# Kernel optimization log

Hardware: AMD Instinct MI355X
Metric: run time of the kernel (lower is better)

The kernel has to match this reference:

```python
import jax, jax.numpy as jnp
import numpy as np

# Qwen3-0.6B-like config; 4 equal-length requests flattened into [R*S, H]
L, R, S, H = 2, 4, 1024, 1024
NH, NKV, DH = 16, 8, 128
FF = 3072
EPS = 1e-6
THETA = 1e6
SCALE = 0.02  # weight init scale to keep activations sane


def setup_inputs() -> dict:
    key = jax.random.key(0)
    ks = jax.random.split(key, 8)
    return {
        "hidden_states": jax.random.normal(ks[0], (R * S, H), jnp.float32),
        "Wq": jax.random.normal(ks[1], (L, H, NH * DH), jnp.float32) * SCALE,
        "Wk": jax.random.normal(ks[2], (L, H, NKV * DH), jnp.float32) * SCALE,
        "Wv": jax.random.normal(ks[3], (L, H, NKV * DH), jnp.float32) * SCALE,
        "Wo": jax.random.normal(ks[4], (L, NH * DH, H), jnp.float32) * SCALE,
        "q_norm_w": jnp.ones((L, DH), jnp.float32),
        "k_norm_w": jnp.ones((L, DH), jnp.float32),
        "ln1_w": jnp.ones((L, H), jnp.float32),
        "ln2_w": jnp.ones((L, H), jnp.float32),
        "Wg": jax.random.normal(ks[5], (L, H, FF), jnp.float32) * SCALE,
        "Wu": jax.random.normal(ks[6], (L, H, FF), jnp.float32) * SCALE,
        "Wd": jax.random.normal(ks[7], (L, FF, H), jnp.float32) * SCALE,
        "final_norm_w": jnp.ones((H,), jnp.float32),
    }


def _rms(x, w):
    return x * jax.lax.rsqrt(jnp.mean(x * x, axis=-1, keepdims=True) + EPS) * w


def _rope_tables():
    inv_freq = 1.0 / (THETA ** (jnp.arange(0, DH, 2, dtype=jnp.float32) / DH))
    pos = jnp.arange(S, dtype=jnp.float32)  # per-request positions 0..S-1 (prefill)
    freqs = pos[:, None] * inv_freq[None, :]        # [S, DH/2]
    emb = jnp.concatenate([freqs, freqs], axis=-1)  # [S, DH]
    return jnp.cos(emb), jnp.sin(emb)


def _rotate_half(x):
    x1, x2 = jnp.split(x, 2, axis=-1)
    return jnp.concatenate([-x2, x1], axis=-1)


def _apply_rope(x, cos, sin):
    # x: [R, heads, S, DH]; cos/sin: [S, DH]
    c = cos[None, None]
    s = sin[None, None]
    return x * c + _rotate_half(x) * s


def reference(hidden_states, Wq, Wk, Wv, Wo, q_norm_w, k_norm_w, ln1_w, ln2_w,
              Wg, Wu, Wd, final_norm_w):
    cos, sin = _rope_tables()
    causal = jnp.tril(jnp.ones((S, S), dtype=bool))  # per-request causal mask
    neg = jnp.finfo(hidden_states.dtype).min
    scaling = 1.0 / jnp.sqrt(jnp.asarray(DH, hidden_states.dtype))

    x = hidden_states
    for l in range(L):
        # --- attention block ---
        residual = x
        h = _rms(x, ln1_w[l])                       # [R*S, H]
        q = (h @ Wq[l]).reshape(R, S, NH, DH)
        k = (h @ Wk[l]).reshape(R, S, NKV, DH)
        v = (h @ Wv[l]).reshape(R, S, NKV, DH)
        q = _rms(q, q_norm_w[l]).transpose(0, 2, 1, 3)   # [R, NH, S, DH]
        k = _rms(k, k_norm_w[l]).transpose(0, 2, 1, 3)   # [R, NKV, S, DH]
        v = v.transpose(0, 2, 1, 3)                      # [R, NKV, S, DH]
        q = _apply_rope(q, cos, sin)
        k = _apply_rope(k, cos, sin)
        # GQA: repeat KV heads
        rep = NH // NKV
        k = jnp.repeat(k, rep, axis=1)
        v = jnp.repeat(v, rep, axis=1)
        scores = jnp.einsum('rhqd,rhkd->rhqk', q, k) * scaling
        scores = jnp.where(causal[None, None], scores, neg)
        attn = jax.nn.softmax(scores, axis=-1)
        o = jnp.einsum('rhqk,rhkd->rhqd', attn, v)       # [R, NH, S, DH]
        o = o.transpose(0, 2, 1, 3).reshape(R * S, NH * DH)
        x = residual + o @ Wo[l]
        # --- MLP block ---
        residual = x
        h = _rms(x, ln2_w[l])
        x = residual + (jax.nn.silu(h @ Wg[l]) * (h @ Wu[l])) @ Wd[l]
    return _rms(x, final_norm_w)
```

## Files before the change

kernel.cpp:

```cpp
#include <hip/hip_runtime.h>
#include <hip/hip_bf16.h>

typedef __bf16 bf16;
typedef __bf16 bf16x8 __attribute__((ext_vector_type(8)));
typedef float f32x4 __attribute__((ext_vector_type(4)));

#define DEVINL __device__ __forceinline__

constexpr int L_ = 2, R_ = 4, S_ = 1024, H_ = 1024;
constexpr int NH_ = 16, NKV_ = 8, DH_ = 128;
constexpr int FF_ = 3072;
constexpr int T_ = R_ * S_;

DEVINL void gload16(const bf16* g, bf16* l) {
    __builtin_amdgcn_global_load_lds(
        (const __attribute__((address_space(1))) void*)g,
        (__attribute__((address_space(3))) void*)l, 16, 0, 0);
}

__global__ void rope_tables_kernel(float* __restrict__ cosb, float* __restrict__ sinb) {
    int s = blockIdx.x;
    int i = threadIdx.x;
    float inv = __expf(-(float)i * (1.0f / 64.0f) * 13.815510557964274f);
    float f = (float)s * inv;
    cosb[s * 64 + i] = cosf(f);
    sinb[s * 64 + i] = sinf(f);
}

template <bool OUT_BF16>
__global__ __launch_bounds__(256) void rmsnorm_kernel(const float* __restrict__ x,
                                                      const float* __restrict__ w,
                                                      void* __restrict__ out) {
    int row = blockIdx.x;
    const float* xr = x + (size_t)row * H_;
    int t = threadIdx.x;
    float v[4];
    float ss = 0.f;
#pragma unroll
    for (int j = 0; j < 4; ++j) {
        v[j] = xr[t + 256 * j];
        ss += v[j] * v[j];
    }
#pragma unroll
    for (int off = 32; off; off >>= 1) ss += __shfl_xor(ss, off);
    __shared__ float part[4];
    if ((t & 63) == 0) part[t >> 6] = ss;
    __syncthreads();
    ss = part[0] + part[1] + part[2] + part[3];
    float r = rsqrtf(ss * (1.0f / (float)H_) + 1e-6f);
#pragma unroll
    for (int j = 0; j < 4; ++j) {
        int c = t + 256 * j;
        float o = v[j] * r * w[c];
        if constexpr (OUT_BF16)
            ((bf16*)out)[(size_t)row * H_ + c] = (bf16)o;
        else
            ((float*)out)[(size_t)row * H_ + c] = o;
    }
}

__global__ __launch_bounds__(256) void transpose_cast_kernel(const float* __restrict__ in,
                                                             bf16* __restrict__ out,
                                                             int Rk, int Cn, int mode) {
    __shared__ float tile[32][33];
    int c0 = blockIdx.x * 32, r0 = blockIdx.y * 32;
    int t = threadIdx.x;
    int tc = t & 31, tr = t >> 5;
#pragma unroll
    for (int i = 0; i < 4; ++i) {
        int r = tr + i * 8;
        tile[r][tc] = in[(size_t)(r0 + r) * Cn + c0 + tc];
    }
    __syncthreads();
#pragma unroll
    for (int i = 0; i < 4; ++i) {
        int c = c0 + tr + i * 8;
        int n = (mode == 0) ? c : (((c >> 4) << 5) + ((mode == 2) ? 16 : 0) + (c & 15));
        out[(size_t)n * Rk + r0 + tc] = (bf16)tile[tc][tr + i * 8];
    }
}

__global__ __launch_bounds__(256) void vt_kernel(const bf16* __restrict__ qkv,
                                                 bf16* __restrict__ vt) {
    __shared__ bf16 tile[32][34];
    int s0 = blockIdx.x * 32, c0 = blockIdx.y * 32, r = blockIdx.z;
    int t = threadIdx.x, tc = t & 31, tr = t >> 5;
#pragma unroll
    for (int i = 0; i < 4; ++i) {
        int s = tr + i * 8;
        tile[s][tc] = qkv[(size_t)(r * 1024 + s0 + s) * 4096 + 3072 + c0 + tc];
    }
    __syncthreads();
#pragma unroll
    for (int i = 0; i < 4; ++i) {
        int c = tr + i * 8;
        vt[((size_t)(r * 1024 + c0 + c)) * 1024 + s0 + tc] = tile[tc][c];
    }
}

template <int EPI>
__global__ __launch_bounds__(512, 4) void gemmP_kernel(const bf16* __restrict__ A,
                                                       const bf16* __restrict__ Bt,
                                                       void* __restrict__ out,
                                                       int M, int N, int K) {
    __shared__ bf16 lds[36864];
    const int NT = K >> 5;
    int nbn = N >> 8;
    int nwg = (M >> 7) * nbn;
    int id = blockIdx.x;
    int sid = (id & 7) * (nwg >> 3) + (id >> 3);
    int bm = (sid / nbn) << 7, bn = (sid % nbn) << 8;
    int t = threadIdx.x, lane = t & 63, w = t >> 6;
    int wm = w >> 2, wn = w & 3;
    int hi = lane >> 4, f = lane & 15;

    int srow = t >> 2;
    int ssc = (t & 3) ^ ((srow >> 1) & 3);
    const bf16* aSrc = A + (size_t)(bm + srow) * K + (ssc << 3);
    const bf16* b0Src = Bt + (size_t)(bn + srow) * K + (ssc << 3);
    const bf16* b1Src = Bt + (size_t)(bn + 128 + srow) * K + (ssc << 3);

    f32x4 acc[4][4] = {};

    auto stage = [&](int tt, int sb) {
        gload16(aSrc + tt * 32, lds + sb * 4096 + w * 512);
        gload16(b0Src + tt * 32, lds + 12288 + sb * 8192 + w * 512);
        gload16(b1Src + tt * 32, lds + 12288 + sb * 8192 + 4096 + w * 512);
    };

    stage(0, 0);
    stage(1, 1);
    asm volatile("s_waitcnt vmcnt(3)" ::: "memory");
    __builtin_amdgcn_s_barrier();

    int cb = 0;
    for (int tau = 0; tau < NT; ++tau) {
        const bf16* aB = lds + cb * 4096;
        const bf16* bB = lds + 12288 + cb * 8192;
        if (tau + 2 < NT) stage(tau + 2, (cb == 0) ? 2 : cb - 1);
        bf16x8 af[4], bfv[4];
#pragma unroll
        for (int mf = 0; mf < 4; ++mf) {
            int row = wm * 64 + mf * 16 + f;
            af[mf] = *(const bf16x8*)(aB + row * 32 + ((hi ^ ((row >> 1) & 3)) << 3));
        }
#pragma unroll
        for (int nf = 0; nf < 4; ++nf) {
            int row = wn * 64 + nf * 16 + f;
            bfv[nf] = *(const bf16x8*)(bB + row * 32 + ((hi ^ ((row >> 1) & 3)) << 3));
        }
        __builtin_amdgcn_s_setprio(1);
#pragma unroll
        for (int mf = 0; mf < 4; ++mf)
#pragma unroll
            for (int nf = 0; nf < 4; ++nf)
                acc[mf][nf] = __builtin_amdgcn_mfma_f32_16x16x32_bf16(af[mf], bfv[nf],
                                                                      acc[mf][nf], 0, 0, 0);
        __builtin_amdgcn_s_setprio(0);
        if (tau < NT - 2)
            asm volatile("s_waitcnt vmcnt(3)" ::: "memory");
        else
            asm volatile("s_waitcnt vmcnt(0)" ::: "memory");
        __builtin_amdgcn_s_barrier();
        cb = (cb == 2) ? 0 : cb + 1;
    }

    int rb = bm + wm * 64 + hi * 4;
#pragma unroll
    for (int mf = 0; mf < 4; ++mf) {
        if constexpr (EPI == 5) {
#pragma unroll
            for (int p = 0; p < 2; ++p) {
                int col = ((bn + wn * 64) >> 1) + p * 16 + f;
#pragma unroll
                for (int g = 0; g < 4; ++g) {
                    float gv = acc[mf][2 * p][g], uv = acc[mf][2 * p + 1][g];
                    float sv = gv / (1.0f + __expf(-gv));
                    ((bf16*)out)[(size_t)(rb + mf * 16 + g) * (N / 2) + col] = (bf16)(sv * uv);
                }
            }
        } else {
            int cb2 = bn + wn * 64 + f;
#pragma unroll
            for (int nf = 0; nf < 4; ++nf)
#pragma unroll
                for (int g = 0; g < 4; ++g)
                    ((bf16*)out)[(size_t)(rb + mf * 16 + g) * N + cb2 + nf * 16] =
                        (bf16)acc[mf][nf][g];
        }
    }
}

template <int EPI, int BM>
__global__ __launch_bounds__(256) void gemm_kernel(const bf16* __restrict__ A,
                                                   const bf16* __restrict__ Bt,
                                                   void* __restrict__ out,
                                                   const float* __restrict__ res,
                                                   int M, int N, int K) {
    constexpr int MF = BM / 32;
    __shared__ bf16 Al[BM * 32];
    __shared__ bf16 Bl[128 * 32];
    int gx = gridDim.x;
    int nwg = gx * gridDim.y;
    int id = blockIdx.y * gx + blockIdx.x;
    int sid = (id & 7) * (nwg >> 3) + (id >> 3);
    int bm = (sid / gx) * BM, bn = (sid % gx) * 128;
    int t = threadIdx.x;
    int lane = t & 63, w = t >> 6;
    int wr = w >> 1, wc = w & 1;
    f32x4 acc[MF][4] = {};

    int srow = t >> 2, scol = (t & 3) * 8;
    const bf16* Ap = A + (size_t)(bm + srow) * K + scol;
    const bf16* Bp = Bt + (size_t)(bn + srow) * K + scol;
    bf16* Adst = Al + w * 512;
    bf16* Bdst = Bl + w * 512;

    int kl = (lane >> 4) * 8;
    int rm = wr * (BM / 2) + (lane & 15);
    int rn = wc * 64 + (lane & 15);

    for (int k0 = 0; k0 < K; k0 += 32) {
        __syncthreads();
        gload16(Ap, Adst);
        if constexpr (BM == 128) gload16(Ap + (size_t)64 * K, Adst + 2048);
        gload16(Bp, Bdst);
        gload16(Bp + (size_t)64 * K, Bdst + 2048);
        Ap += 32;
        Bp += 32;
        __syncthreads();
        bf16x8 af[MF], bfv[4];
#pragma unroll
        for (int m = 0; m < MF; ++m) af[m] = *(const bf16x8*)(Al + (rm + m * 16) * 32 + kl);
#pragma unroll
        for (int n = 0; n < 4; ++n) bfv[n] = *(const bf16x8*)(Bl + (rn + n * 16) * 32 + kl);
#pragma unroll
        for (int m = 0; m < MF; ++m)
#pragma unroll
            for (int n = 0; n < 4; ++n)
                acc[m][n] = __builtin_amdgcn_mfma_f32_16x16x32_bf16(af[m], bfv[n], acc[m][n], 0, 0, 0);
    }

    int f = lane & 15;
    int rbase = bm + wr * (BM / 2) + ((lane >> 4) << 2);
    int cbase = bn + wc * 64 + f;
#pragma unroll
    for (int m = 0; m < MF; ++m) {
#pragma unroll
        for (int n = 0; n < 4; ++n) {
#pragma unroll
            for (int g = 0; g < 4; ++g) {
                int row = rbase + m * 16 + g;
                size_t idx = (size_t)row * N + cbase + n * 16;
                ((float*)out)[idx] = acc[m][n][g] + res[idx];
            }
        }
    }
}

DEVINL void head_norm_rope(const bf16* __restrict__ src, const float* __restrict__ w,
                           const float* __restrict__ cosb, const float* __restrict__ sinb,
                           int s, int ln, bf16* __restrict__ dst) {
    float x0 = (float)src[ln], x1 = (float)src[ln + 32];
    float x2 = (float)src[ln + 64], x3 = (float)src[ln + 96];
    float ss = x0 * x0 + x1 * x1 + x2 * x2 + x3 * x3;
#pragma unroll
    for (int off = 16; off; off >>= 1) ss += __shfl_xor(ss, off);
    float rr = rsqrtf(ss * (1.0f / 128.0f) + 1e-6f);
    float n0 = x0 * rr * w[ln], n1 = x1 * rr * w[ln + 32];
    float n2 = x2 * rr * w[ln + 64], n3 = x3 * rr * w[ln + 96];
    float c0 = cosb[s * 64 + ln], c1 = cosb[s * 64 + ln + 32];
    float s0 = sinb[s * 64 + ln], s1 = sinb[s * 64 + ln + 32];
    dst[ln] = (bf16)(n0 * c0 - n2 * s0);
    dst[ln + 32] = (bf16)(n1 * c1 - n3 * s1);
    dst[ln + 64] = (bf16)(n2 * c0 + n0 * s0);
    dst[ln + 96] = (bf16)(n3 * c1 + n1 * s1);
}

__global__ __launch_bounds__(256) void qkv_post_kernel(const bf16* __restrict__ qkv,
                                                       const float* __restrict__ qw,
                                                       const float* __restrict__ kw,
                                                       const float* __restrict__ cosb,
                                                       const float* __restrict__ sinb,
                                                       bf16* __restrict__ qo,
                                                       bf16* __restrict__ ko) {
    int tok = blockIdx.x;
    int r = tok >> 10, s = tok & 1023;
    int t = threadIdx.x;
    int g = t >> 5;
    int ln = t & 31;
    const bf16* row = qkv + (size_t)tok * 4096;
#pragma unroll
    for (int hh = 0; hh < 2; ++hh) {
        int h = g + hh * 8;
        head_norm_rope(row + h * 128, qw, cosb, sinb, s, ln,
                       qo + ((size_t)(r * NH_ + h) * S_ + s) * 128);
    }
    head_norm_rope(row + 2048 + g * 128, kw, cosb, sinb, s, ln,
                   ko + ((size_t)(r * NKV_ + g) * S_ + s) * 128);
}

__global__ __launch_bounds__(256, 2) void flash_kernel(const bf16* __restrict__ q,
                                                       const bf16* __restrict__ k,
                                                       const bf16* __restrict__ vt,
                                                       bf16* __restrict__ out) {
    __shared__ bf16 Kl[64 * 128];
    __shared__ bf16 Vl[128 * 64];
    __shared__ bf16 Pl[4][32][72];
    int bid = blockIdx.x;
    int grp = bid & 63, slot = bid >> 6;
    int strip = (slot < 4) ? (7 - slot) : (slot - 4);
    int h = 2 * (grp & 7) + ((grp >> 3) & 1);
    int r = grp >> 4;
    int kvh = h >> 1;

    int t = threadIdx.x, lane = t & 63, w = t >> 6;
    int arow = lane & 15, hi = lane >> 4;
    int a7 = arow & 7;
    int grow = hi * 4;
    int qbase = strip * 128 + w * 32;

    const bf16* qp = q + ((size_t)(r * NH_ + h) * S_ + qbase) * 128;
    bf16x8 qf[2][4];
#pragma unroll
    for (int m = 0; m < 2; ++m)
#pragma unroll
        for (int kc = 0; kc < 4; ++kc)
            qf[m][kc] = *(const bf16x8*)(qp + (size_t)(m * 16 + arow) * 128 + kc * 32 + hi * 8);

    const bf16* kp = k + (size_t)(r * NKV_ + kvh) * S_ * 128;
    const bf16* vp = vt + (size_t)(r * NKV_ + kvh) * 128 * S_;

    int krow0 = t >> 4, kc16 = t & 15;
    int vrow0 = t >> 3, vc16 = t & 7;

    f32x4 ao[2][8] = {};
    float mrow[2][4], lrow[2][4];
#pragma unroll
    for (int m = 0; m < 2; ++m)
#pragma unroll
        for (int g = 0; g < 4; ++g) { mrow[m][g] = -1e30f; lrow[m][g] = 0.f; }
    const float scale = 0.08838834764831845f;

    int nt = 2 * (strip + 1);
    bf16x8 krs[4], vrs[4];
#pragma unroll
    for (int i = 0; i < 4; ++i)
        krs[i] = *(const bf16x8*)(kp + (size_t)(krow0 + 16 * i) * 128 + kc16 * 8);
#pragma unroll
    for (int i = 0; i < 4; ++i)
        vrs[i] = *(const bf16x8*)(vp + (size_t)(vrow0 + 32 * i) * S_ + vc16 * 8);

    for (int it = 0; it < nt; ++it) {
        int kv0 = it * 64;
        __syncthreads();
#pragma unroll
        for (int i = 0; i < 4; ++i) {
            int row = krow0 + 16 * i;
            *(bf16x8*)(&Kl[row * 128 + ((kc16 ^ (row & 7)) * 8)]) = krs[i];
        }
#pragma unroll
        for (int i = 0; i < 4; ++i) {
            int row = vrow0 + 32 * i;
            *(bf16x8*)(&Vl[row * 64 + ((vc16 ^ (row & 7)) * 8)]) = vrs[i];
        }
        __syncthreads();
        if (it + 1 < nt) {
            int kvn = kv0 + 64;
#pragma unroll
            for (int i = 0; i < 4; ++i)
                krs[i] = *(const bf16x8*)(kp + (size_t)(kvn + krow0 + 16 * i) * 128 + kc16 * 8);
#pragma unroll
            for (int i = 0; i < 4; ++i)
                vrs[i] = *(const bf16x8*)(vp + (size_t)(vrow0 + 32 * i) * S_ + kvn + vc16 * 8);
        }
        f32x4 sc[2][4];
#pragma unroll
        for (int m = 0; m < 2; ++m)
#pragma unroll
            for (int n = 0; n < 4; ++n) sc[m][n] = (f32x4){0.f, 0.f, 0.f, 0.f};
#pragma unroll
        for (int n = 0; n < 4; ++n) {
            int krw = n * 16 + arow;
#pragma unroll
            for (int kc = 0; kc < 4; ++kc) {
                bf16x8 kf = *(const bf16x8*)(&Kl[krw * 128 + (((kc * 4 + hi) ^ a7) * 8)]);
                sc[0][n] = __builtin_amdgcn_mfma_f32_16x16x32_bf16(qf[0][kc], kf, sc[0][n], 0, 0, 0);
                sc[1][n] = __builtin_amdgcn_mfma_f32_16x16x32_bf16(qf[1][kc], kf, sc[1][n], 0, 0, 0);
            }
        }
#pragma unroll
        for (int m = 0; m < 2; ++m) {
            float pm[4][4];
            bool msk = (kv0 + 64 > qbase + m * 16);
#pragma unroll
            for (int n = 0; n < 4; ++n)
#pragma unroll
                for (int g = 0; g < 4; ++g) {
                    float sval = sc[m][n][g] * scale;
                    if (msk && (kv0 + n * 16 + arow > qbase + m * 16 + grow + g)) sval = -1e30f;
                    pm[n][g] = sval;
                }
            float mx[4], sf[4], rs[4];
#pragma unroll
            for (int g = 0; g < 4; ++g)
                mx[g] = fmaxf(fmaxf(pm[0][g], pm[1][g]), fmaxf(pm[2][g], pm[3][g]));
#pragma unroll
            for (int off = 8; off; off >>= 1)
#pragma unroll
                for (int g = 0; g < 4; ++g) mx[g] = fmaxf(mx[g], __shfl_xor(mx[g], off));
#pragma unroll
            for (int g = 0; g < 4; ++g) {
                float mnew = fmaxf(mrow[m][g], mx[g]);
                sf[g] = __expf(mrow[m][g] - mnew);
                mrow[m][g] = mnew;
            }
#pragma unroll
            for (int n = 0; n < 4; ++n)
#pragma unroll
                for (int g = 0; g < 4; ++g) pm[n][g] = __expf(pm[n][g] - mrow[m][g]);
#pragma unroll
            for (int g = 0; g < 4; ++g) rs[g] = pm[0][g] + pm[1][g] + pm[2][g] + pm[3][g];
#pragma unroll
            for (int off = 8; off; off >>= 1)
#pragma unroll
                for (int g = 0; g < 4; ++g) rs[g] += __shfl_xor(rs[g], off);
#pragma unroll
            for (int g = 0; g < 4; ++g) lrow[m][g] = lrow[m][g] * sf[g] + rs[g];
#pragma unroll
            for (int c = 0; c < 8; ++c)
#pragma unroll
                for (int g = 0; g < 4; ++g) ao[m][c][g] *= sf[g];
#pragma unroll
            for (int n = 0; n < 4; ++n)
#pragma unroll
                for (int g = 0; g < 4; ++g)
                    Pl[w][m * 16 + grow + g][n * 16 + arow] = (bf16)pm[n][g];
        }
        bf16x8 pf[2][2];
#pragma unroll
        for (int m = 0; m < 2; ++m)
#pragma unroll
            for (int ks = 0; ks < 2; ++ks)
                pf[m][ks] = *(const bf16x8*)(&Pl[w][m * 16 + arow][ks * 32 + hi * 8]);
#pragma unroll
        for (int c = 0; c < 8; ++c) {
            int vrw = c * 16 + arow;
#pragma unroll
            for (int ks = 0; ks < 2; ++ks) {
                bf16x8 vf = *(const bf16x8*)(&Vl[vrw * 64 + (((ks * 4 + hi) ^ a7) * 8)]);
                ao[0][c] = __builtin_amdgcn_mfma_f32_16x16x32_bf16(pf[0][ks], vf, ao[0][c], 0, 0, 0);
                ao[1][c] = __builtin_amdgcn_mfma_f32_16x16x32_bf16(pf[1][ks], vf, ao[1][c], 0, 0, 0);
            }
        }
    }
#pragma unroll
    for (int m = 0; m < 2; ++m)
#pragma unroll
        for (int c = 0; c < 8; ++c)
#pragma unroll
            for (int g = 0; g < 4; ++g) {
                int rq = qbase + m * 16 + grow + g;
                out[(size_t)(r * S_ + rq) * 2048 + h * 128 + c * 16 + arow] =
                    (bf16)(ao[m][c][g] / lrow[m][g]);
            }
}

extern "C" void kernel_launch(void* const* d_in, const int* in_sizes, int n_in,
                              void* d_out, int out_size, void* d_ws, size_t ws_size,
                              hipStream_t stream) {
    const float* hidden = (const float*)d_in[0];
    const float* Wq = (const float*)d_in[1];
    const float* Wk = (const float*)d_in[2];
    const float* Wv = (const float*)d_in[3];
    const float* Wo = (const float*)d_in[4];
    const float* qnw = (const float*)d_in[5];
    const float* knw = (const float*)d_in[6];
    const float* ln1 = (const float*)d_in[7];
    const float* ln2 = (const float*)d_in[8];
    const float* Wg = (const float*)d_in[9];
    const float* Wu = (const float*)d_in[10];
    const float* Wd = (const float*)d_in[11];
    const float* fnw = (const float*)d_in[12];
    float* out = (float*)d_out;

    char* ws = (char*)d_ws;
    size_t off = 0;
    auto alloc = [&](size_t bytes) -> char* {
        char* p = ws + off;
        off += (bytes + 255) & ~(size_t)255;
        return p;
    };
    float* cosb = (float*)alloc((size_t)S_ * 64 * 4);
    float* sinb = (float*)alloc((size_t)S_ * 64 * 4);
    float* x_ws = (float*)alloc((size_t)T_ * H_ * 4);
    bf16* hbuf = (bf16*)alloc((size_t)T_ * H_ * 2);
    bf16* qkv = (bf16*)alloc((size_t)T_ * 4096 * 2);
    bf16* act = qkv;
    bf16* qb = (bf16*)alloc((size_t)R_ * NH_ * S_ * 128 * 2);
    bf16* kb = (bf16*)alloc((size_t)R_ * NKV_ * S_ * 128 * 2);
    bf16* vtb = (bf16*)alloc((size_t)R_ * NKV_ * 128 * S_ * 2);
    bf16* attn = (bf16*)alloc((size_t)T_ * 2048 * 2);
    bf16* wqkv_t = (bf16*)alloc((size_t)4096 * 1024 * 2);
    bf16* wo_t = (bf16*)alloc((size_t)1024 * 2048 * 2);
    bf16* wgu_t = (bf16*)alloc((size_t)6144 * 1024 * 2);
    bf16* wd_t = (bf16*)alloc((size_t)1024 * 3072 * 2);

    rope_tables_kernel<<<S_, 64, 0, stream>>>(cosb, sinb);

    const float* xin = hidden;
    for (int l = 0; l < L_; ++l) {
        transpose_cast_kernel<<<dim3(2048 / 32, 1024 / 32), 256, 0, stream>>>(
            Wq + (size_t)l * H_ * 2048, wqkv_t, 1024, 2048, 0);
        transpose_cast_kernel<<<dim3(1024 / 32, 1024 / 32), 256, 0, stream>>>(
            Wk + (size_t)l * H_ * 1024, wqkv_t + (size_t)2048 * 1024, 1024, 1024, 0);
        transpose_cast_kernel<<<dim3(1024 / 32, 1024 / 32), 256, 0, stream>>>(
            Wv + (size_t)l * H_ * 1024, wqkv_t + (size_t)3072 * 1024, 1024, 1024, 0);
        transpose_cast_kernel<<<dim3(1024 / 32, 2048 / 32), 256, 0, stream>>>(
            Wo + (size_t)l * 2048 * 1024, wo_t, 2048, 1024, 0);
        transpose_cast_kernel<<<dim3(3072 / 32, 1024 / 32), 256, 0, stream>>>(
            Wg + (size_t)l * H_ * 3072, wgu_t, 1024, 3072, 1);
        transpose_cast_kernel<<<dim3(3072 / 32, 1024 / 32), 256, 0, stream>>>(
            Wu + (size_t)l * H_ * 3072, wgu_t, 1024, 3072, 2);
        transpose_cast_kernel<<<dim3(1024 / 32, 3072 / 32), 256, 0, stream>>>(
            Wd + (size_t)l * 3072 * 1024, wd_t, 3072, 1024, 0);

        rmsnorm_kernel<true><<<T_, 256, 0, stream>>>(xin, ln1 + (size_t)l * H_, hbuf);
        gemmP_kernel<1><<<512, 512, 0, stream>>>(hbuf, wqkv_t, qkv, 4096, 4096, 1024);
        qkv_post_kernel<<<T_, 256, 0, stream>>>(qkv, qnw + (size_t)l * 128, knw + (size_t)l * 128,
                                                cosb, sinb, qb, kb);
        vt_kernel<<<dim3(32, 32, 4), 256, 0, stream>>>(qkv, vtb);
        flash_kernel<<<512, 256, 0, stream>>>(qb, kb, vtb, attn);
        gemm_kernel<4, 64><<<dim3(8, 64), 256, 0, stream>>>(attn, wo_t, x_ws, xin,
                                                            4096, 1024, 2048);
        rmsnorm_kernel<true><<<T_, 256, 0, stream>>>(x_ws, ln2 + (size_t)l * H_, hbuf);
        gemmP_kernel<5><<<768, 512, 0, stream>>>(hbuf, wgu_t, act, 4096, 6144, 1024);
        gemm_kernel<4, 64><<<dim3(8, 64), 256, 0, stream>>>(act, wd_t, x_ws, x_ws,
                                                            4096, 1024, 3072);
        xin = x_ws;
    }
    rmsnorm_kernel<false><<<T_, 256, 0, stream>>>(x_ws, fnw, out);
}
```

Before: 617.4 us.

## Add 256x256 GEMM for QKV projection and remap tiles per XCD column slices

Adds a gemmQ kernel with 256x256 output tiles, triple-buffered LDS and 8x4 MFMA fragments per wave, and uses it for the QKV projection in place of the 128x256 gemmP. The larger tile raises arithmetic intensity per LDS load, at the cost of more registers and LDS, which limits occupancy to 2 workgroups. All GEMM kernels also change their block-to-tile mapping so each XCD owns a contiguous slice of N columns, with M iterated inside it. This is meant to improve L2 reuse of the weight tiles within each XCD.

```diff
diff --git a/kernel.cpp b/kernel.cpp
--- a/kernel.cpp
+++ b/kernel.cpp
@@ -99,17 +99,98 @@
 }
 
 template <int EPI>
+__global__ __launch_bounds__(512, 2) void gemmQ_kernel(const bf16* __restrict__ A,
+                                                       const bf16* __restrict__ Bt,
+                                                       void* __restrict__ out,
+                                                       int M, int N, int K) {
+    __shared__ bf16 lds[49152];
+    const int NT = K >> 5;
+    int nbm = M >> 8, nbn = N >> 8;
+    int slice = nbn >> 3;
+    int id = blockIdx.x;
+    int xcd = id & 7, wi = id >> 3;
+    int bm = (wi % nbm) << 8, bn = (xcd * slice + wi / nbm) << 8;
+    int t = threadIdx.x, lane = t & 63, w = t >> 6;
+    int wm = w >> 2, wn = w & 3;
+    int hi = lane >> 4, f = lane & 15;
+
+    int srow = t >> 2;
+    int ssc = (t & 3) ^ ((srow >> 1) & 3);
+    const bf16* a0 = A + (size_t)(bm + srow) * K + (ssc << 3);
+    const bf16* a1 = A + (size_t)(bm + 128 + srow) * K + (ssc << 3);
+    const bf16* b0 = Bt + (size_t)(bn + srow) * K + (ssc << 3);
+    const bf16* b1 = Bt + (size_t)(bn + 128 + srow) * K + (ssc << 3);
+
+    f32x4 acc[8][4] = {};
+
+    auto stage = [&](int tt, int sb) {
+        gload16(a0 + tt * 32, lds + sb * 8192 + w * 512);
+        gload16(a1 + tt * 32, lds + sb * 8192 + 4096 + w * 512);
+        gload16(b0 + tt * 32, lds + 24576 + sb * 8192 + w * 512);
+        gload16(b1 + tt * 32, lds + 24576 + sb * 8192 + 4096 + w * 512);
+    };
+
+    stage(0, 0);
+    stage(1, 1);
+    asm volatile("s_waitcnt vmcnt(4)" ::: "memory");
+    __builtin_amdgcn_s_barrier();
+
+    int cb = 0;
+    for (int tau = 0; tau < NT; ++tau) {
+        const bf16* aB = lds + cb * 8192;
+        const bf16* bB = lds + 24576 + cb * 8192;
+        if (tau + 2 < NT) stage(tau + 2, (cb == 0) ? 2 : cb - 1);
+        bf16x8 af[8], bfv[4];
+#pragma unroll
+        for (int mf = 0; mf < 8; ++mf) {
+            int row = wm * 128 + mf * 16 + f;
+            af[mf] = *(const bf16x8*)(aB + row * 32 + ((hi ^ ((row >> 1) & 3)) << 3));
+        }
+#pragma unroll
+        for (int nf = 0; nf < 4; ++nf) {
+            int row = wn * 64 + nf * 16 + f;
+            bfv[nf] = *(const bf16x8*)(bB + row * 32 + ((hi ^ ((row >> 1) & 3)) << 3));
+        }
+        __builtin_amdgcn_s_setprio(1);
+#pragma unroll
+        for (int mf = 0; mf < 8; ++mf)
+#pragma unroll
+            for (int nf = 0; nf < 4; ++nf)
+                acc[mf][nf] = __builtin_amdgcn_mfma_f32_16x16x32_bf16(af[mf], bfv[nf],
+                                                                      acc[mf][nf], 0, 0, 0);
+        __builtin_amdgcn_s_setprio(0);
+        if (tau < NT - 2)
+            asm volatile("s_waitcnt vmcnt(4)" ::: "memory");
+        else
+            asm volatile("s_waitcnt vmcnt(0)" ::: "memory");
+        __builtin_amdgcn_s_barrier();
+        cb = (cb == 2) ? 0 : cb + 1;
+    }
+
+    int rb = bm + wm * 128 + hi * 4;
+    int cb2 = bn + wn * 64 + f;
+#pragma unroll
+    for (int mf = 0; mf < 8; ++mf)
+#pragma unroll
+        for (int nf = 0; nf < 4; ++nf)
+#pragma unroll
+            for (int g = 0; g < 4; ++g)
+                ((bf16*)out)[(size_t)(rb + mf * 16 + g) * N + cb2 + nf * 16] =
+                    (bf16)acc[mf][nf][g];
+}
+
+template <int EPI>
 __global__ __launch_bounds__(512, 4) void gemmP_kernel(const bf16* __restrict__ A,
                                                        const bf16* __restrict__ Bt,
                                                        void* __restrict__ out,
                                                        int M, int N, int K) {
     __shared__ bf16 lds[36864];
     const int NT = K >> 5;
-    int nbn = N >> 8;
-    int nwg = (M >> 7) * nbn;
+    int nbm = M >> 7, nbn = N >> 8;
+    int slice = nbn >> 3;
     int id = blockIdx.x;
-    int sid = (id & 7) * (nwg >> 3) + (id >> 3);
-    int bm = (sid / nbn) << 7, bn = (sid % nbn) << 8;
+    int xcd = id & 7, wi = id >> 3;
+    int bm = (wi % nbm) << 7, bn = (xcd * slice + wi / nbm) << 8;
     int t = threadIdx.x, lane = t & 63, w = t >> 6;
     int wm = w >> 2, wn = w & 3;
     int hi = lane >> 4, f = lane & 15;
@@ -201,10 +282,11 @@
     __shared__ bf16 Al[BM * 32];
     __shared__ bf16 Bl[128 * 32];
     int gx = gridDim.x;
-    int nwg = gx * gridDim.y;
+    int nbm = gridDim.y;
     int id = blockIdx.y * gx + blockIdx.x;
-    int sid = (id & 7) * (nwg >> 3) + (id >> 3);
-    int bm = (sid / gx) * BM, bn = (sid % gx) * 128;
+    int slice = gx >> 3;
+    int xcd = id & 7, wi = id >> 3;
+    int bm = (wi % nbm) * BM, bn = (xcd * slice + wi / nbm) * 128;
     int t = threadIdx.x;
     int lane = t & 63, w = t >> 6;
     int wr = w >> 1, wc = w & 1;
@@ -526,7 +608,7 @@
             Wd + (size_t)l * 3072 * 1024, wd_t, 3072, 1024, 0);
 
         rmsnorm_kernel<true><<<T_, 256, 0, stream>>>(xin, ln1 + (size_t)l * H_, hbuf);
-        gemmP_kernel<1><<<512, 512, 0, stream>>>(hbuf, wqkv_t, qkv, 4096, 4096, 1024);
+        gemmQ_kernel<1><<<256, 512, 0, stream>>>(hbuf, wqkv_t, qkv, 4096, 4096, 1024);
         qkv_post_kernel<<<T_, 256, 0, stream>>>(qkv, qnw + (size_t)l * 128, knw + (size_t)l * 128,
                                                 cosb, sinb, qb, kb);
         vt_kernel<<<dim3(32, 32, 4), 256, 0, stream>>>(qkv, vtb);
```

After: 616.2 us. Within noise of the previous version (-0.2%).
